# Optimization experiments

Measured on AMD Instinct MI355X. Metric: run time of the kernel, lower is better.

## Reference

```python
import jax, jax.numpy as jnp
import numpy as np

N, C, K, H = 100000, 128, 16, 128
MIX_IN = 2 * C + 1 + C   # x, mean_feat, boundary_score, coord_embed
GATE_IN = 2 * C + 1


def _mlp2(x, w1, b1, w2, b2):
    # Linear -> GELU(exact) -> Linear (dropout=0 at eval)
    return jax.nn.gelu(x @ w1 + b1, approximate=False) @ w2 + b2


def setup_inputs() -> dict:
    key = jax.random.key(0)
    ks = jax.random.split(key, 16)
    s = 0.02
    return {
        "feats": jax.random.normal(ks[0], (N, C), jnp.float32),
        "points": jax.random.normal(ks[1], (N, 3), jnp.float32),
        "neighbors": jax.random.randint(ks[2], (N, K), 0, N, jnp.int64),
        "ln_g": jnp.ones((C,), jnp.float32),
        "ln_b": jnp.zeros((C,), jnp.float32),
        "cp_w1": jax.random.normal(ks[3], (3, H), jnp.float32) * s,
        "cp_b1": jnp.zeros((H,), jnp.float32),
        "cp_w2": jax.random.normal(ks[4], (H, C), jnp.float32) * s,
        "cp_b2": jnp.zeros((C,), jnp.float32),
        "bd_w1": jax.random.normal(ks[5], (2, H), jnp.float32) * s,
        "bd_b1": jnp.zeros((H,), jnp.float32),
        "bd_w2": jax.random.normal(ks[6], (H, 1), jnp.float32) * s,
        "bd_b2": jnp.zeros((1,), jnp.float32),
        "mix_w1": jax.random.normal(ks[7], (MIX_IN, H), jnp.float32) * s,
        "mix_b1": jnp.zeros((H,), jnp.float32),
        "mix_w2": jax.random.normal(ks[8], (H, C), jnp.float32) * s,
        "mix_b2": jnp.zeros((C,), jnp.float32),
        "gate_w1": jax.random.normal(ks[9], (GATE_IN, H), jnp.float32) * s,
        "gate_b1": jnp.zeros((H,), jnp.float32),
        "gate_w2": jax.random.normal(ks[10], (H, C), jnp.float32) * s,
        "gate_b2": jnp.zeros((C,), jnp.float32),
        "out_w": jax.random.normal(ks[11], (C, C), jnp.float32) * s,
        "out_b": jnp.zeros((C,), jnp.float32),
    }


def _forward(feats, points, neighbors, ln_g, ln_b, cp_w1, cp_b1, cp_w2, cp_b2,
             bd_w1, bd_b1, bd_w2, bd_b2, mix_w1, mix_b1, mix_w2, mix_b2,
             gate_w1, gate_b1, gate_w2, gate_b2, out_w, out_b):
    n = feats.shape[0]
    # LayerNorm (eps=1e-5, torch default)
    mu = feats.mean(-1, keepdims=True)
    var = jnp.mean((feats - mu) ** 2, -1, keepdims=True)
    x = (feats - mu) * jax.lax.rsqrt(var + 1e-5) * ln_g + ln_b

    # sanitize neighbors
    valid = ((neighbors >= 0) & (neighbors < n)).astype(x.dtype)  # [N,K]
    safe = jnp.clip(neighbors, 0, n - 1)

    neigh_feats = x[safe]        # [N,K,C]
    neigh_points = points[safe]  # [N,K,3]
    denom = jnp.maximum(valid.sum(1, keepdims=True), 1.0)  # [N,1]
    w = valid[..., None]
    mean_feat = (neigh_feats * w).sum(1) / denom    # [N,C]
    mean_point = (neigh_points * w).sum(1) / denom  # [N,3]

    feat_diff = jnp.linalg.norm(x - mean_feat, axis=-1, keepdims=True)       # [N,1]
    coord_diff = jnp.linalg.norm(points - mean_point, axis=-1, keepdims=True)

    boundary = jax.nn.sigmoid(_mlp2(jnp.concatenate([feat_diff, coord_diff], -1),
                                    bd_w1, bd_b1, bd_w2, bd_b2))  # [N,1]

    # normalize points globally
    centered = points - points.mean(0, keepdims=True)
    scale = jnp.maximum(jnp.abs(centered).max(0, keepdims=True), 1e-6)
    coord_embed = _mlp2(centered / scale, cp_w1, cp_b1, cp_w2, cp_b2)  # [N,C]

    refined = _mlp2(jnp.concatenate([x, mean_feat, boundary, coord_embed], -1),
                    mix_w1, mix_b1, mix_w2, mix_b2)
    gate = jax.nn.sigmoid(_mlp2(jnp.concatenate([x, mean_feat, boundary], -1),
                                gate_w1, gate_b1, gate_w2, gate_b2))
    refined = (gate * refined) @ out_w + out_b
    return feats + refined


def reference(feats, points, neighbors, ln_g, ln_b, cp_w1, cp_b1, cp_w2, cp_b2,
              bd_w1, bd_b1, bd_w2, bd_b2, mix_w1, mix_b1, mix_w2, mix_b2,
              gate_w1, gate_b1, gate_w2, gate_b2, out_w, out_b):
    return _forward(feats, points, neighbors, ln_g, ln_b, cp_w1, cp_b1, cp_w2, cp_b2,
                    bd_w1, bd_b1, bd_w2, bd_b2, mix_w1, mix_b1, mix_w2, mix_b2,
                    gate_w1, gate_b1, gate_w2, gate_b2, out_w, out_b)
```

## Files before the change

### kernel.cpp

```cpp
#include <hip/hip_runtime.h>
#include <math.h>

constexpr int C    = 128;
constexpr int K    = 16;
constexpr int H    = 128;
constexpr int NB2  = 256;
constexpr int WPTS = 32;
constexpr int PB   = 128;
constexpr int HSU  = 68;

constexpr int WT_MIX   = 0;
constexpr int WT_GATE  = 49152;
constexpr int WT_CP2   = 81920;
constexpr int WT_MIX2  = 98304;
constexpr int WT_GATE2 = 114688;
constexpr int WT_OUT   = 131072;
constexpr int WT_TOTAL = 147456;

typedef __attribute__((ext_vector_type(8))) short short8;
typedef __attribute__((ext_vector_type(4))) short short4v;
typedef __attribute__((ext_vector_type(4))) float f32x4;

__device__ __forceinline__ short f2bf(float f) {
    unsigned u = __float_as_uint(f);
    unsigned r = (u + 0x7fffu + ((u >> 16) & 1u)) >> 16;
    return (short)r;
}
__device__ __forceinline__ float bflo(unsigned v) { return __uint_as_float(v << 16); }
__device__ __forceinline__ float bfhi(unsigned v) { return __uint_as_float(v & 0xffff0000u); }
__device__ __forceinline__ float rcpf(float v) { return __builtin_amdgcn_rcpf(v); }

__device__ __forceinline__ float gelu_f(float x) {
    float a = fabsf(x) * 0.70710678118654752440f;
    float t = rcpf(1.0f + 0.3275911f * a);
    float p = t * (0.254829592f + t * (-0.284496736f + t * (1.421413741f
            + t * (-1.453152027f + t * 1.061405429f))));
    float e = __expf(-a * a);
    float er = 1.0f - p * e;
    return 0.5f * x * (1.0f + copysignf(er, x));
}
__device__ __forceinline__ float sigm(float v) { return rcpf(1.0f + __expf(-v)); }

__global__ __launch_bounds__(256) void prep_wt(
    const float* __restrict__ mix_w1, const float* __restrict__ gate_w1,
    const float* __restrict__ cp_w2,  const float* __restrict__ mix_w2,
    const float* __restrict__ gate_w2, const float* __restrict__ out_w,
    short* __restrict__ wt, unsigned* __restrict__ xb_zero_row)
{
    int b = blockIdx.x;
    if (b == 36) {
        if (threadIdx.x < 64) xb_zero_row[threadIdx.x] = 0u;
        return;
    }
    const float* src; int off; int c; bool skip256 = false;
    if (b < 12)      { src = mix_w1;  off = WT_MIX;   c = b;      skip256 = true; }
    else if (b < 20) { src = gate_w1; off = WT_GATE;  c = b - 12; }
    else if (b < 24) { src = cp_w2;   off = WT_CP2;   c = b - 20; }
    else if (b < 28) { src = mix_w2;  off = WT_MIX2;  c = b - 24; }
    else if (b < 32) { src = gate_w2; off = WT_GATE2; c = b - 28; }
    else             { src = out_w;   off = WT_OUT;   c = b - 32; }
    for (int ii = 0; ii < 16; ++ii) {
        int e = ii * 256 + threadIdx.x;
        int j = e & 7, l = (e >> 3) & 63, t = e >> 9;
        int k = c * 32 + ((l >> 4) * 8) + j;
        int nn = t * 16 + (l & 15);
        int kk = (skip256 && k >= 256) ? k + 1 : k;
        wt[off + c * 4096 + e] = f2bf(src[kk * C + nn]);
    }
}

__global__ __launch_bounds__(256) void ln_kernel(
    const float* __restrict__ feats, const float* __restrict__ g,
    const float* __restrict__ b, unsigned* __restrict__ xb, int n)
{
    const int lane = threadIdx.x & 63;
    const int wave = threadIdx.x >> 6;
    const int i = blockIdx.x * 4 + wave;
    if (i >= n) return;
    const float2 f = *(const float2*)(feats + i * C + 2 * lane);
    float s = f.x + f.y;
    #pragma unroll
    for (int o = 32; o > 0; o >>= 1) s += __shfl_xor(s, o, 64);
    const float mu = s * (1.0f / C);
    const float d0 = f.x - mu, d1 = f.y - mu;
    float v = d0 * d0 + d1 * d1;
    #pragma unroll
    for (int o = 32; o > 0; o >>= 1) v += __shfl_xor(v, o, 64);
    const float rs = rsqrtf(v * (1.0f / C) + 1e-5f);
    const float x0 = d0 * rs * g[2 * lane] + b[2 * lane];
    const float x1 = d1 * rs * g[2 * lane + 1] + b[2 * lane + 1];
    unsigned pk = (unsigned short)f2bf(x0) | ((unsigned)(unsigned short)f2bf(x1) << 16);
    xb[(size_t)i * 64 + lane] = pk;
}

__global__ __launch_bounds__(256) void pstat_partial(
    const float* __restrict__ pts, float* __restrict__ partial, int n)
{
    __shared__ float sm[256];
    const int tid = threadIdx.x;
    float s[3] = {0, 0, 0};
    float mn[3] = {1e30f, 1e30f, 1e30f};
    float mx[3] = {-1e30f, -1e30f, -1e30f};
    for (int i = blockIdx.x * blockDim.x + tid; i < n; i += gridDim.x * blockDim.x) {
        #pragma unroll
        for (int c = 0; c < 3; ++c) {
            float v = pts[i * 3 + c];
            s[c] += v; mn[c] = fminf(mn[c], v); mx[c] = fmaxf(mx[c], v);
        }
    }
    for (int q = 0; q < 9; ++q) {
        float v = (q < 3) ? s[q] : (q < 6) ? mn[q - 3] : mx[q - 6];
        sm[tid] = v;
        __syncthreads();
        for (int o = 128; o > 0; o >>= 1) {
            if (tid < o) {
                float a = sm[tid], c = sm[tid + o];
                sm[tid] = (q < 3) ? a + c : (q < 6) ? fminf(a, c) : fmaxf(a, c);
            }
            __syncthreads();
        }
        if (tid == 0) partial[blockIdx.x * 9 + q] = sm[0];
        __syncthreads();
    }
}

__global__ __launch_bounds__(256) void pstat_final(
    const float* __restrict__ partial, float* __restrict__ stats, int n)
{
    __shared__ float sm[256];
    const int tid = threadIdx.x;
    for (int q = 0; q < 9; ++q) {
        float v = partial[tid * 9 + q];
        sm[tid] = v;
        __syncthreads();
        for (int o = 128; o > 0; o >>= 1) {
            if (tid < o) {
                float a = sm[tid], c = sm[tid + o];
                sm[tid] = (q < 3) ? a + c : (q < 6) ? fminf(a, c) : fmaxf(a, c);
            }
            __syncthreads();
        }
        if (tid == 0) sm[q] = sm[0];
        __syncthreads();
    }
    if (tid < 3) {
        float mean = sm[tid] / (float)n;
        float scale = fmaxf(fmaxf(sm[6 + tid] - mean, mean - sm[3 + tid]), 1e-6f);
        stats[tid] = mean;
        stats[3 + tid] = scale;
    }
}

__global__ __launch_bounds__(256, 2) void main_kernel(
    const unsigned* __restrict__ xb, const float* __restrict__ feats,
    const float* __restrict__ points, const int* __restrict__ neighbors,
    const float* __restrict__ stats, const short* __restrict__ wt,
    const float* __restrict__ cp_w1, const float* __restrict__ cp_b1,
    const float* __restrict__ cp_b2,
    const float* __restrict__ bd_w1, const float* __restrict__ bd_b1,
    const float* __restrict__ bd_w2, const float* __restrict__ bd_b2,
    const float* __restrict__ mix_w1, const float* __restrict__ mix_b1,
    const float* __restrict__ mix_b2,
    const float* __restrict__ gate_w1, const float* __restrict__ gate_b1,
    const float* __restrict__ gate_b2,
    const float* __restrict__ out_b,
    float* __restrict__ out, int n)
{
    __shared__ __align__(16) char lds[74752];
    unsigned* mf_s  = (unsigned*)lds;
    unsigned* hid_s = (unsigned*)(lds + 34816);
    float* denom_s  = (float*)(lds + 69632);
    float* mp_s     = denom_s + 128;
    float* pts_s    = mp_s + 384;
    float* cd_s     = pts_s + 512;
    float* bd_s     = cd_s + 128;

    const int tid  = threadIdx.x;
    const int lane = tid & 63;
    const int w    = tid >> 6;
    const int m16  = lane & 15;
    const int h4   = lane >> 4;
    const int i0   = blockIdx.x * PB;
    const int wv32 = w * WPTS;
    const int i0w  = i0 + wv32;
    int* nb_w = (int*)(hid_s + (size_t)wv32 * HSU);

    {
        const int p0 = lane >> 2;
        const int jb = 4 * (lane & 3);
        const int r0 = min(i0w + p0, n - 1);
        const int r1 = min(i0w + 16 + p0, n - 1);
        const int4 A0 = *(const int4*)(neighbors + r0 * K + jb);
        const int4 A1 = *(const int4*)(neighbors + r1 * K + jb);

        const bool b00 = (unsigned)A0.x < (unsigned)n, b01 = (unsigned)A0.y < (unsigned)n;
        const bool b02 = (unsigned)A0.z < (unsigned)n, b03 = (unsigned)A0.w < (unsigned)n;
        const bool b10 = (unsigned)A1.x < (unsigned)n, b11 = (unsigned)A1.y < (unsigned)n;
        const bool b12 = (unsigned)A1.z < (unsigned)n, b13 = (unsigned)A1.w < (unsigned)n;

        *(int4*)&nb_w[4 * lane]       = make_int4(b00 ? A0.x : n, b01 ? A0.y : n,
                                                  b02 ? A0.z : n, b03 ? A0.w : n);
        *(int4*)&nb_w[256 + 4 * lane] = make_int4(b10 ? A1.x : n, b11 ? A1.y : n,
                                                  b12 ? A1.z : n, b13 ? A1.w : n);

        float c0 = (float)((int)b00 + (int)b01 + (int)b02 + (int)b03);
        float c1 = (float)((int)b10 + (int)b11 + (int)b12 + (int)b13);
        c0 += __shfl_xor(c0, 1, 64); c0 += __shfl_xor(c0, 2, 64);
        c1 += __shfl_xor(c1, 1, 64); c1 += __shfl_xor(c1, 2, 64);
        const float d0 = fmaxf(c0, 1.0f), d1 = fmaxf(c1, 1.0f);
        if ((lane & 3) == 0) {
            denom_s[wv32 + p0]      = d0;
            denom_s[wv32 + 16 + p0] = d1;
        }
        const float rd0 = rcpf(d0), rd1 = rcpf(d1);

        const int q00 = b00 ? A0.x : 0, q01 = b01 ? A0.y : 0, q02 = b02 ? A0.z : 0, q03 = b03 ? A0.w : 0;
        const int q10 = b10 ? A1.x : 0, q11 = b11 ? A1.y : 0, q12 = b12 ? A1.z : 0, q13 = b13 ? A1.w : 0;
        const float f00 = b00 ? 1.f : 0.f, f01 = b01 ? 1.f : 0.f, f02 = b02 ? 1.f : 0.f, f03 = b03 ? 1.f : 0.f;
        const float f10 = b10 ? 1.f : 0.f, f11 = b11 ? 1.f : 0.f, f12 = b12 ? 1.f : 0.f, f13 = b13 ? 1.f : 0.f;
        #pragma unroll
        for (int c = 0; c < 3; ++c) {
            float s0 = f00 * points[q00 * 3 + c] + f01 * points[q01 * 3 + c]
                     + f02 * points[q02 * 3 + c] + f03 * points[q03 * 3 + c];
            float s1 = f10 * points[q10 * 3 + c] + f11 * points[q11 * 3 + c]
                     + f12 * points[q12 * 3 + c] + f13 * points[q13 * 3 + c];
            s0 += __shfl_xor(s0, 1, 64); s0 += __shfl_xor(s0, 2, 64);
            s1 += __shfl_xor(s1, 1, 64); s1 += __shfl_xor(s1, 2, 64);
            if ((lane & 3) == 0) {
                mp_s[(wv32 + p0) * 3 + c]      = s0 * rd0;
                mp_s[(wv32 + 16 + p0) * 3 + c] = s1 * rd1;
            }
        }
    }

    if (lane < WPTS) {
        const int ipp = min(i0w + lane, n - 1);
        const float pv0 = points[ipp * 3 + 0];
        const float pv1 = points[ipp * 3 + 1];
        const float pv2 = points[ipp * 3 + 2];
        const float e0 = pv0 - mp_s[(wv32 + lane) * 3 + 0];
        const float e1 = pv1 - mp_s[(wv32 + lane) * 3 + 1];
        const float e2 = pv2 - mp_s[(wv32 + lane) * 3 + 2];
        cd_s[wv32 + lane] = sqrtf(e0 * e0 + e1 * e1 + e2 * e2);
        pts_s[(wv32 + lane) * 4 + 0] = (pv0 - stats[0]) * rcpf(stats[3]);
        pts_s[(wv32 + lane) * 4 + 1] = (pv1 - stats[1]) * rcpf(stats[4]);
        pts_s[(wv32 + lane) * 4 + 2] = (pv2 - stats[2]) * rcpf(stats[5]);
    }

    const float bw_fa = bd_w1[lane],     bw_fb = bd_w1[64 + lane];
    const float bw_ca = bd_w1[H + lane], bw_cb = bd_w1[H + 64 + lane];
    const float bb1a  = bd_b1[lane],     bb1b  = bd_b1[64 + lane];
    const float bw2a  = bd_w2[lane],     bw2b  = bd_w2[64 + lane];
    const float bb2   = bd_b2[0];

    for (int p = 0; p < WPTS; ++p) {
        const int* nbp = nb_w + p * K;
        float fx = 0.0f, fy = 0.0f;
        #pragma unroll
        for (int k = 0; k < K; ++k) {
            const int idx = nbp[k];
            const unsigned v = xb[(size_t)idx * 64 + lane];
            fx += bflo(v); fy += bfhi(v);
        }
        const float rden = rcpf(denom_s[wv32 + p]);
        const float mfx = fx * rden, mfy = fy * rden;
        mf_s[(wv32 + p) * HSU + lane] =
            (unsigned)(unsigned short)f2bf(mfx) | ((unsigned)(unsigned short)f2bf(mfy) << 16);
        const int ipp = min(i0w + p, n - 1);
        const unsigned xv = xb[(size_t)ipp * 64 + lane];
        const float dx = bflo(xv) - mfx, dy = bfhi(xv) - mfy;
        float ss = dx * dx + dy * dy;
        #pragma unroll
        for (int o = 32; o > 0; o >>= 1) ss += __shfl_xor(ss, o, 64);
        const float fd = sqrtf(ss);
        const float cd = cd_s[wv32 + p];
        float s = gelu_f(fd * bw_fa + cd * bw_ca + bb1a) * bw2a
                + gelu_f(fd * bw_fb + cd * bw_cb + bb1b) * bw2b;
        #pragma unroll
        for (int o = 32; o > 0; o >>= 1) s += __shfl_xor(s, o, 64);
        if (lane == 0) bd_s[wv32 + p] = sigm(s + bb2);
    }

    const int pr0 = wv32 + m16, pr1 = wv32 + 16 + m16;
    const int ig0 = i0 + pr0,   ig1 = i0 + pr1;
    const int ip0 = min(ig0, n - 1), ip1 = min(ig1, n - 1);
    const unsigned* xr0  = xb + (size_t)ip0 * 64;
    const unsigned* xr1  = xb + (size_t)ip1 * 64;
    const unsigned* mfr0 = mf_s + pr0 * HSU;
    const unsigned* mfr1 = mf_s + pr1 * HSU;
    unsigned* hr0 = hid_s + pr0 * HSU;
    unsigned* hr1 = hid_s + pr1 * HSU;

    {
        const float px0 = pts_s[pr0 * 4], py0 = pts_s[pr0 * 4 + 1], pz0 = pts_s[pr0 * 4 + 2];
        const float px1 = pts_s[pr1 * 4], py1 = pts_s[pr1 * 4 + 1], pz1 = pts_s[pr1 * 4 + 2];
        f32x4 a0[8], a1[8];
        #pragma unroll
        for (int t = 0; t < 8; ++t) { a0[t] = (f32x4)0.0f; a1[t] = (f32x4)0.0f; }
        #pragma unroll
        for (int c = 0; c < 4; ++c) {
            short8 af0, af1;
            #pragma unroll
            for (int j = 0; j < 8; ++j) {
                const int hh = c * 32 + h4 * 8 + j;
                const float wa = cp_w1[hh], wb = cp_w1[H + hh], wc2 = cp_w1[2 * H + hh];
                const float bb = cp_b1[hh];
                af0[j] = f2bf(gelu_f(bb + px0 * wa + py0 * wb + pz0 * wc2));
                af1[j] = f2bf(gelu_f(bb + px1 * wa + py1 * wb + pz1 * wc2));
            }
            const short* wcp = wt + WT_CP2 + c * 4096 + lane * 8;
            #pragma unroll
            for (int t = 0; t < 8; ++t) {
                const short8 wf = *(const short8*)(wcp + t * 512);
                a0[t] = __builtin_amdgcn_mfma_f32_16x16x32_bf16(wf, af0, a0[t], 0, 0, 0);
                a1[t] = __builtin_amdgcn_mfma_f32_16x16x32_bf16(wf, af1, a1[t], 0, 0, 0);
            }
        }
        #pragma unroll
        for (int t = 0; t < 8; ++t) {
            const f32x4 bb = *(const f32x4*)(cp_b2 + t * 16 + h4 * 4);
            const f32x4 v0 = a0[t] + bb, v1 = a1[t] + bb;
            short4v pk0, pk1;
            #pragma unroll
            for (int r = 0; r < 4; ++r) { pk0[r] = f2bf(v0[r]); pk1[r] = f2bf(v1[r]); }
            *(short4v*)((short*)hr0 + t * 16 + h4 * 4) = pk0;
            *(short4v*)((short*)hr1 + t * 16 + h4 * 4) = pk1;
        }
    }

    const float bdp0 = bd_s[pr0], bdp1 = bd_s[pr1];

    {
        f32x4 a0[8], a1[8];
        #pragma unroll
        for (int t = 0; t < 8; ++t) { a0[t] = (f32x4)0.0f; a1[t] = (f32x4)0.0f; }
        #pragma unroll
        for (int c = 0; c < 12; ++c) {
            short8 af0, af1;
            if (c < 4) {
                af0 = *(const short8*)(xr0 + c * 16 + h4 * 4);
                af1 = *(const short8*)(xr1 + c * 16 + h4 * 4);
            } else if (c < 8) {
                af0 = *(const short8*)(mfr0 + (c - 4) * 16 + h4 * 4);
                af1 = *(const short8*)(mfr1 + (c - 4) * 16 + h4 * 4);
            } else {
                af0 = *(const short8*)(hr0 + (c - 8) * 16 + h4 * 4);
                af1 = *(const short8*)(hr1 + (c - 8) * 16 + h4 * 4);
            }
            const short* wmc = wt + WT_MIX + c * 4096 + lane * 8;
            #pragma unroll
            for (int t = 0; t < 8; ++t) {
                const short8 wf = *(const short8*)(wmc + t * 512);
                a0[t] = __builtin_amdgcn_mfma_f32_16x16x32_bf16(wf, af0, a0[t], 0, 0, 0);
                a1[t] = __builtin_amdgcn_mfma_f32_16x16x32_bf16(wf, af1, a1[t], 0, 0, 0);
            }
        }
        #pragma unroll
        for (int t = 0; t < 8; ++t) {
            const int col = t * 16 + h4 * 4;
            const f32x4 wb = *(const f32x4*)(mix_w1 + 256 * C + col);
            const f32x4 bb = *(const f32x4*)(mix_b1 + col);
            const f32x4 v0 = a0[t] + bdp0 * wb + bb;
            const f32x4 v1 = a1[t] + bdp1 * wb + bb;
            short4v pk0, pk1;
            #pragma unroll
            for (int r = 0; r < 4; ++r) { pk0[r] = f2bf(gelu_f(v0[r])); pk1[r] = f2bf(gelu_f(v1[r])); }
            *(short4v*)((short*)hr0 + col) = pk0;
            *(short4v*)((short*)hr1 + col) = pk1;
        }
    }

    f32x4 rf0[8], rf1[8];
    {
        #pragma unroll
        for (int t = 0; t < 8; ++t) { rf0[t] = (f32x4)0.0f; rf1[t] = (f32x4)0.0f; }
        #pragma unroll
        for (int c = 0; c < 4; ++c) {
            const short8 af0 = *(const short8*)(hr0 + c * 16 + h4 * 4);
            const short8 af1 = *(const short8*)(hr1 + c * 16 + h4 * 4);
            const short* wmc = wt + WT_MIX2 + c * 4096 + lane * 8;
            #pragma unroll
            for (int t = 0; t < 8; ++t) {
                const short8 wf = *(const short8*)(wmc + t * 512);
                rf0[t] = __builtin_amdgcn_mfma_f32_16x16x32_bf16(wf, af0, rf0[t], 0, 0, 0);
                rf1[t] = __builtin_amdgcn_mfma_f32_16x16x32_bf16(wf, af1, rf1[t], 0, 0, 0);
            }
        }
        #pragma unroll
        for (int t = 0; t < 8; ++t) {
            const f32x4 bb = *(const f32x4*)(mix_b2 + t * 16 + h4 * 4);
            rf0[t] += bb; rf1[t] += bb;
        }
    }

    {
        f32x4 a0[8], a1[8];
        #pragma unroll
        for (int t = 0; t < 8; ++t) { a0[t] = (f32x4)0.0f; a1[t] = (f32x4)0.0f; }
        #pragma unroll
        for (int c = 0; c < 8; ++c) {
            short8 af0, af1;
            if (c < 4) {
                af0 = *(const short8*)(xr0 + c * 16 + h4 * 4);
                af1 = *(const short8*)(xr1 + c * 16 + h4 * 4);
            } else {
                af0 = *(const short8*)(mfr0 + (c - 4) * 16 + h4 * 4);
                af1 = *(const short8*)(mfr1 + (c - 4) * 16 + h4 * 4);
            }
            const short* wgc = wt + WT_GATE + c * 4096 + lane * 8;
            #pragma unroll
            for (int t = 0; t < 8; ++t) {
                const short8 wf = *(const short8*)(wgc + t * 512);
                a0[t] = __builtin_amdgcn_mfma_f32_16x16x32_bf16(wf, af0, a0[t], 0, 0, 0);
                a1[t] = __builtin_amdgcn_mfma_f32_16x16x32_bf16(wf, af1, a1[t], 0, 0, 0);
            }
        }
        #pragma unroll
        for (int t = 0; t < 8; ++t) {
            const int col = t * 16 + h4 * 4;
            const f32x4 wb = *(const f32x4*)(gate_w1 + 256 * C + col);
            const f32x4 bb = *(const f32x4*)(gate_b1 + col);
            const f32x4 v0 = a0[t] + bdp0 * wb + bb;
            const f32x4 v1 = a1[t] + bdp1 * wb + bb;
            short4v pk0, pk1;
            #pragma unroll
            for (int r = 0; r < 4; ++r) { pk0[r] = f2bf(gelu_f(v0[r])); pk1[r] = f2bf(gelu_f(v1[r])); }
            *(short4v*)((short*)hr0 + col) = pk0;
            *(short4v*)((short*)hr1 + col) = pk1;
        }
    }

    {
        f32x4 a0[8], a1[8];
        #pragma unroll
        for (int t = 0; t < 8; ++t) { a0[t] = (f32x4)0.0f; a1[t] = (f32x4)0.0f; }
        #pragma unroll
        for (int c = 0; c < 4; ++c) {
            const short8 af0 = *(const short8*)(hr0 + c * 16 + h4 * 4);
            const short8 af1 = *(const short8*)(hr1 + c * 16 + h4 * 4);
            const short* wgc = wt + WT_GATE2 + c * 4096 + lane * 8;
            #pragma unroll
            for (int t = 0; t < 8; ++t) {
                const short8 wf = *(const short8*)(wgc + t * 512);
                a0[t] = __builtin_amdgcn_mfma_f32_16x16x32_bf16(wf, af0, a0[t], 0, 0, 0);
                a1[t] = __builtin_amdgcn_mfma_f32_16x16x32_bf16(wf, af1, a1[t], 0, 0, 0);
            }
        }
        #pragma unroll
        for (int t = 0; t < 8; ++t) {
            const int col = t * 16 + h4 * 4;
            const f32x4 bb = *(const f32x4*)(gate_b2 + col);
            short4v pk0, pk1;
            #pragma unroll
            for (int r = 0; r < 4; ++r) {
                pk0[r] = f2bf(sigm(a0[t][r] + bb[r]) * rf0[t][r]);
                pk1[r] = f2bf(sigm(a1[t][r] + bb[r]) * rf1[t][r]);
            }
            *(short4v*)((short*)hr0 + col) = pk0;
            *(short4v*)((short*)hr1 + col) = pk1;
        }
    }

    {
        f32x4 a0[8], a1[8];
        #pragma unroll
        for (int t = 0; t < 8; ++t) { a0[t] = (f32x4)0.0f; a1[t] = (f32x4)0.0f; }
        #pragma unroll
        for (int c = 0; c < 4; ++c) {
            const short8 af0 = *(const short8*)(hr0 + c * 16 + h4 * 4);
            const short8 af1 = *(const short8*)(hr1 + c * 16 + h4 * 4);
            const short* woc = wt + WT_OUT + c * 4096 + lane * 8;
            #pragma unroll
            for (int t = 0; t < 8; ++t) {
                const short8 wf = *(const short8*)(woc + t * 512);
                a0[t] = __builtin_amdgcn_mfma_f32_16x16x32_bf16(wf, af0, a0[t], 0, 0, 0);
                a1[t] = __builtin_amdgcn_mfma_f32_16x16x32_bf16(wf, af1, a1[t], 0, 0, 0);
            }
        }
        #pragma unroll
        for (int t = 0; t < 8; ++t) {
            const int col = t * 16 + h4 * 4;
            const f32x4 bb = *(const f32x4*)(out_b + col);
            const f32x4 fv0 = *(const f32x4*)(feats + (size_t)ip0 * C + col);
            const f32x4 fv1 = *(const f32x4*)(feats + (size_t)ip1 * C + col);
            const f32x4 v0 = a0[t] + bb + fv0;
            const f32x4 v1 = a1[t] + bb + fv1;
            if (ig0 < n) *(f32x4*)(out + (size_t)ig0 * C + col) = v0;
            if (ig1 < n) *(f32x4*)(out + (size_t)ig1 * C + col) = v1;
        }
    }
}

extern "C" void kernel_launch(void* const* d_in, const int* in_sizes, int n_in,
                              void* d_out, int out_size, void* d_ws, size_t ws_size,
                              hipStream_t stream)
{
    const float* feats     = (const float*)d_in[0];
    const float* points    = (const float*)d_in[1];
    const int*   neighbors = (const int*)d_in[2];
    const float* ln_g      = (const float*)d_in[3];
    const float* ln_b      = (const float*)d_in[4];
    const float* cp_w1     = (const float*)d_in[5];
    const float* cp_b1     = (const float*)d_in[6];
    const float* cp_w2     = (const float*)d_in[7];
    const float* cp_b2     = (const float*)d_in[8];
    const float* bd_w1     = (const float*)d_in[9];
    const float* bd_b1     = (const float*)d_in[10];
    const float* bd_w2     = (const float*)d_in[11];
    const float* bd_b2     = (const float*)d_in[12];
    const float* mix_w1    = (const float*)d_in[13];
    const float* mix_b1    = (const float*)d_in[14];
    const float* mix_w2    = (const float*)d_in[15];
    const float* mix_b2    = (const float*)d_in[16];
    const float* gate_w1   = (const float*)d_in[17];
    const float* gate_b1   = (const float*)d_in[18];
    const float* gate_w2   = (const float*)d_in[19];
    const float* gate_b2   = (const float*)d_in[20];
    const float* out_w     = (const float*)d_in[21];
    const float* out_b     = (const float*)d_in[22];
    float* out = (float*)d_out;
    (void)n_in; (void)out_size; (void)ws_size;

    const int n = in_sizes[0] / C;

    char* base = (char*)d_ws;
    unsigned* xb   = (unsigned*)base;
    short* wt      = (short*)(base + (size_t)(n + 1) * 256);
    float* partial = (float*)((char*)wt + (size_t)WT_TOTAL * 2);
    float* stats   = partial + NB2 * 9;

    prep_wt<<<37, 256, 0, stream>>>(mix_w1, gate_w1, cp_w2, mix_w2, gate_w2, out_w,
                                    wt, xb + (size_t)n * 64);
    ln_kernel<<<(n + 3) / 4, 256, 0, stream>>>(feats, ln_g, ln_b, xb, n);
    pstat_partial<<<NB2, 256, 0, stream>>>(points, partial, n);
    pstat_final<<<1, 256, 0, stream>>>(partial, stats, n);
    main_kernel<<<(n + PB - 1) / PB, 256, 0, stream>>>(
        xb, feats, points, neighbors, stats, wt,
        cp_w1, cp_b1, cp_b2, bd_w1, bd_b1, bd_w2, bd_b2,
        mix_w1, mix_b1, mix_b2, gate_w1, gate_b1, gate_b2,
        out_b, out, n);
}
```

Before: 375.1 us.

## Gather neighbor features in FP8 e5m2 with prefetch and padded point array

LayerNorm now also writes an 8-bit e5m2 copy of the normalized features, and the neighbor-mean gather reads it instead of the bf16 copy. This halves the bytes fetched per neighbor row. The gather loop is restructured so each half-wave handles one point, and the next point's 16 neighbor loads are prefetched into registers while the current point is reduced. Points are also repacked into a padded float4 array so neighbor coordinates come in as single vector loads, and the coordinate-difference computation is folded into the setup. The cost is a much coarser mean_feat (e5m2 has only 2 mantissa bits), which risks tolerance failures, plus higher register pressure from the prefetch buffers.

```diff
diff --git a/kernel.cpp b/kernel.cpp
--- a/kernel.cpp
+++ b/kernel.cpp
@@ -29,6 +29,17 @@
 __device__ __forceinline__ float bflo(unsigned v) { return __uint_as_float(v << 16); }
 __device__ __forceinline__ float bfhi(unsigned v) { return __uint_as_float(v & 0xffff0000u); }
 __device__ __forceinline__ float rcpf(float v) { return __builtin_amdgcn_rcpf(v); }
+
+__device__ __forceinline__ float e5m2f(unsigned b) {
+    union { unsigned short u; _Float16 h; } cv;
+    cv.u = (unsigned short)((b & 0xFFu) << 8);
+    return (float)cv.h;
+}
+__device__ __forceinline__ unsigned f2e5m2(float x) {
+    union { _Float16 h; unsigned short u; } cv;
+    cv.h = (_Float16)x;
+    return ((unsigned)cv.u + 0x7Fu + ((cv.u >> 8) & 1u)) >> 8;
+}
 
 __device__ __forceinline__ float gelu_f(float x) {
     float a = fabsf(x) * 0.70710678118654752440f;
@@ -45,11 +56,27 @@
     const float* __restrict__ mix_w1, const float* __restrict__ gate_w1,
     const float* __restrict__ cp_w2,  const float* __restrict__ mix_w2,
     const float* __restrict__ gate_w2, const float* __restrict__ out_w,
-    short* __restrict__ wt, unsigned* __restrict__ xb_zero_row)
+    const float* __restrict__ points,
+    short* __restrict__ wt, unsigned* __restrict__ xb_zero,
+    unsigned* __restrict__ xg_zero, float* __restrict__ pts4, int n)
 {
     int b = blockIdx.x;
     if (b == 36) {
-        if (threadIdx.x < 64) xb_zero_row[threadIdx.x] = 0u;
+        if (threadIdx.x < 64) xb_zero[threadIdx.x] = 0u;
+        else if (threadIdx.x < 96) xg_zero[threadIdx.x - 64] = 0u;
+        return;
+    }
+    if (b >= 37) {
+        int i = (b - 37) * 256 + threadIdx.x;
+        if (i < n) {
+            pts4[i * 4 + 0] = points[i * 3 + 0];
+            pts4[i * 4 + 1] = points[i * 3 + 1];
+            pts4[i * 4 + 2] = points[i * 3 + 2];
+            pts4[i * 4 + 3] = 0.0f;
+        } else if (i == n) {
+            pts4[i * 4 + 0] = 0.0f; pts4[i * 4 + 1] = 0.0f;
+            pts4[i * 4 + 2] = 0.0f; pts4[i * 4 + 3] = 0.0f;
+        }
         return;
     }
     const float* src; int off; int c; bool skip256 = false;
@@ -71,7 +98,8 @@
 
 __global__ __launch_bounds__(256) void ln_kernel(
     const float* __restrict__ feats, const float* __restrict__ g,
-    const float* __restrict__ b, unsigned* __restrict__ xb, int n)
+    const float* __restrict__ b, unsigned* __restrict__ xb,
+    unsigned short* __restrict__ xg, int n)
 {
     const int lane = threadIdx.x & 63;
     const int wave = threadIdx.x >> 6;
@@ -89,8 +117,10 @@
     const float rs = rsqrtf(v * (1.0f / C) + 1e-5f);
     const float x0 = d0 * rs * g[2 * lane] + b[2 * lane];
     const float x1 = d1 * rs * g[2 * lane + 1] + b[2 * lane + 1];
-    unsigned pk = (unsigned short)f2bf(x0) | ((unsigned)(unsigned short)f2bf(x1) << 16);
-    xb[(size_t)i * 64 + lane] = pk;
+    xb[(size_t)i * 64 + lane] =
+        (unsigned)(unsigned short)f2bf(x0) | ((unsigned)(unsigned short)f2bf(x1) << 16);
+    xg[(size_t)i * 64 + lane] =
+        (unsigned short)(f2e5m2(x0) | (f2e5m2(x1) << 8));
 }
 
 __global__ __launch_bounds__(256) void pstat_partial(
@@ -152,8 +182,9 @@
 }
 
 __global__ __launch_bounds__(256, 2) void main_kernel(
-    const unsigned* __restrict__ xb, const float* __restrict__ feats,
-    const float* __restrict__ points, const int* __restrict__ neighbors,
+    const unsigned* __restrict__ xb, const unsigned* __restrict__ xg,
+    const float* __restrict__ pts4, const float* __restrict__ feats,
+    const int* __restrict__ neighbors,
     const float* __restrict__ stats, const short* __restrict__ wt,
     const float* __restrict__ cp_w1, const float* __restrict__ cp_b1,
     const float* __restrict__ cp_b2,
@@ -166,12 +197,11 @@
     const float* __restrict__ out_b,
     float* __restrict__ out, int n)
 {
-    __shared__ __align__(16) char lds[74752];
+    __shared__ __align__(16) char lds[73216];
     unsigned* mf_s  = (unsigned*)lds;
     unsigned* hid_s = (unsigned*)(lds + 34816);
     float* denom_s  = (float*)(lds + 69632);
-    float* mp_s     = denom_s + 128;
-    float* pts_s    = mp_s + 384;
+    float* pts_s    = denom_s + 128;
     float* cd_s     = pts_s + 512;
     float* bd_s     = cd_s + 128;
 
@@ -190,21 +220,23 @@
         const int jb = 4 * (lane & 3);
         const int r0 = min(i0w + p0, n - 1);
         const int r1 = min(i0w + 16 + p0, n - 1);
-        const int4 A0 = *(const int4*)(neighbors + r0 * K + jb);
-        const int4 A1 = *(const int4*)(neighbors + r1 * K + jb);
-
-        const bool b00 = (unsigned)A0.x < (unsigned)n, b01 = (unsigned)A0.y < (unsigned)n;
-        const bool b02 = (unsigned)A0.z < (unsigned)n, b03 = (unsigned)A0.w < (unsigned)n;
-        const bool b10 = (unsigned)A1.x < (unsigned)n, b11 = (unsigned)A1.y < (unsigned)n;
-        const bool b12 = (unsigned)A1.z < (unsigned)n, b13 = (unsigned)A1.w < (unsigned)n;
-
-        *(int4*)&nb_w[4 * lane]       = make_int4(b00 ? A0.x : n, b01 ? A0.y : n,
-                                                  b02 ? A0.z : n, b03 ? A0.w : n);
-        *(int4*)&nb_w[256 + 4 * lane] = make_int4(b10 ? A1.x : n, b11 ? A1.y : n,
-                                                  b12 ? A1.z : n, b13 ? A1.w : n);
-
-        float c0 = (float)((int)b00 + (int)b01 + (int)b02 + (int)b03);
-        float c1 = (float)((int)b10 + (int)b11 + (int)b12 + (int)b13);
+        const int4 A0 = *(const int4*)(neighbors + (size_t)r0 * K + jb);
+        const int4 A1 = *(const int4*)(neighbors + (size_t)r1 * K + jb);
+
+        const int q00 = ((unsigned)A0.x < (unsigned)n) ? A0.x : n;
+        const int q01 = ((unsigned)A0.y < (unsigned)n) ? A0.y : n;
+        const int q02 = ((unsigned)A0.z < (unsigned)n) ? A0.z : n;
+        const int q03 = ((unsigned)A0.w < (unsigned)n) ? A0.w : n;
+        const int q10 = ((unsigned)A1.x < (unsigned)n) ? A1.x : n;
+        const int q11 = ((unsigned)A1.y < (unsigned)n) ? A1.y : n;
+        const int q12 = ((unsigned)A1.z < (unsigned)n) ? A1.z : n;
+        const int q13 = ((unsigned)A1.w < (unsigned)n) ? A1.w : n;
+
+        *(int4*)&nb_w[4 * lane]       = make_int4(q00, q01, q02, q03);
+        *(int4*)&nb_w[256 + 4 * lane] = make_int4(q10, q11, q12, q13);
+
+        float c0 = (float)((q00 != n) + (q01 != n) + (q02 != n) + (q03 != n));
+        float c1 = (float)((q10 != n) + (q11 != n) + (q12 != n) + (q13 != n));
         c0 += __shfl_xor(c0, 1, 64); c0 += __shfl_xor(c0, 2, 64);
         c1 += __shfl_xor(c1, 1, 64); c1 += __shfl_xor(c1, 2, 64);
         const float d0 = fmaxf(c0, 1.0f), d1 = fmaxf(c1, 1.0f);
@@ -212,73 +244,97 @@
             denom_s[wv32 + p0]      = d0;
             denom_s[wv32 + 16 + p0] = d1;
         }
-        const float rd0 = rcpf(d0), rd1 = rcpf(d1);
-
-        const int q00 = b00 ? A0.x : 0, q01 = b01 ? A0.y : 0, q02 = b02 ? A0.z : 0, q03 = b03 ? A0.w : 0;
-        const int q10 = b10 ? A1.x : 0, q11 = b11 ? A1.y : 0, q12 = b12 ? A1.z : 0, q13 = b13 ? A1.w : 0;
-        const float f00 = b00 ? 1.f : 0.f, f01 = b01 ? 1.f : 0.f, f02 = b02 ? 1.f : 0.f, f03 = b03 ? 1.f : 0.f;
-        const float f10 = b10 ? 1.f : 0.f, f11 = b11 ? 1.f : 0.f, f12 = b12 ? 1.f : 0.f, f13 = b13 ? 1.f : 0.f;
+
+        f32x4 s0 = *(const f32x4*)(pts4 + 4 * q00);
+        s0 += *(const f32x4*)(pts4 + 4 * q01);
+        s0 += *(const f32x4*)(pts4 + 4 * q02);
+        s0 += *(const f32x4*)(pts4 + 4 * q03);
+        f32x4 s1 = *(const f32x4*)(pts4 + 4 * q10);
+        s1 += *(const f32x4*)(pts4 + 4 * q11);
+        s1 += *(const f32x4*)(pts4 + 4 * q12);
+        s1 += *(const f32x4*)(pts4 + 4 * q13);
         #pragma unroll
         for (int c = 0; c < 3; ++c) {
-            float s0 = f00 * points[q00 * 3 + c] + f01 * points[q01 * 3 + c]
-                     + f02 * points[q02 * 3 + c] + f03 * points[q03 * 3 + c];
-            float s1 = f10 * points[q10 * 3 + c] + f11 * points[q11 * 3 + c]
-                     + f12 * points[q12 * 3 + c] + f13 * points[q13 * 3 + c];
-            s0 += __shfl_xor(s0, 1, 64); s0 += __shfl_xor(s0, 2, 64);
-            s1 += __shfl_xor(s1, 1, 64); s1 += __shfl_xor(s1, 2, 64);
-            if ((lane & 3) == 0) {
-                mp_s[(wv32 + p0) * 3 + c]      = s0 * rd0;
-                mp_s[(wv32 + 16 + p0) * 3 + c] = s1 * rd1;
-            }
+            s0[c] += __shfl_xor(s0[c], 1, 64); s0[c] += __shfl_xor(s0[c], 2, 64);
+            s1[c] += __shfl_xor(s1[c], 1, 64); s1[c] += __shfl_xor(s1[c], 2, 64);
+        }
+        if ((lane & 3) == 0) {
+            const float rd0 = rcpf(d0), rd1 = rcpf(d1);
+            const f32x4 pv0 = *(const f32x4*)(pts4 + 4 * r0);
+            const f32x4 pv1 = *(const f32x4*)(pts4 + 4 * r1);
+            const float e00 = pv0[0] - s0[0] * rd0, e01 = pv0[1] - s0[1] * rd0, e02 = pv0[2] - s0[2] * rd0;
+            const float e10 = pv1[0] - s1[0] * rd1, e11 = pv1[1] - s1[1] * rd1, e12 = pv1[2] - s1[2] * rd1;
+            cd_s[wv32 + p0]      = sqrtf(e00 * e00 + e01 * e01 + e02 * e02);
+            cd_s[wv32 + 16 + p0] = sqrtf(e10 * e10 + e11 * e11 + e12 * e12);
         }
     }
 
     if (lane < WPTS) {
         const int ipp = min(i0w + lane, n - 1);
-        const float pv0 = points[ipp * 3 + 0];
-        const float pv1 = points[ipp * 3 + 1];
-        const float pv2 = points[ipp * 3 + 2];
-        const float e0 = pv0 - mp_s[(wv32 + lane) * 3 + 0];
-        const float e1 = pv1 - mp_s[(wv32 + lane) * 3 + 1];
-        const float e2 = pv2 - mp_s[(wv32 + lane) * 3 + 2];
-        cd_s[wv32 + lane] = sqrtf(e0 * e0 + e1 * e1 + e2 * e2);
-        pts_s[(wv32 + lane) * 4 + 0] = (pv0 - stats[0]) * rcpf(stats[3]);
-        pts_s[(wv32 + lane) * 4 + 1] = (pv1 - stats[1]) * rcpf(stats[4]);
-        pts_s[(wv32 + lane) * 4 + 2] = (pv2 - stats[2]) * rcpf(stats[5]);
-    }
-
-    const float bw_fa = bd_w1[lane],     bw_fb = bd_w1[64 + lane];
-    const float bw_ca = bd_w1[H + lane], bw_cb = bd_w1[H + 64 + lane];
-    const float bb1a  = bd_b1[lane],     bb1b  = bd_b1[64 + lane];
-    const float bw2a  = bd_w2[lane],     bw2b  = bd_w2[64 + lane];
-    const float bb2   = bd_b2[0];
-
-    for (int p = 0; p < WPTS; ++p) {
-        const int* nbp = nb_w + p * K;
-        float fx = 0.0f, fy = 0.0f;
+        const f32x4 pv = *(const f32x4*)(pts4 + 4 * ipp);
+        pts_s[(wv32 + lane) * 4 + 0] = (pv[0] - stats[0]) * rcpf(stats[3]);
+        pts_s[(wv32 + lane) * 4 + 1] = (pv[1] - stats[1]) * rcpf(stats[4]);
+        pts_s[(wv32 + lane) * 4 + 2] = (pv[2] - stats[2]) * rcpf(stats[5]);
+    }
+
+    {
+        const int ul   = lane & 31;
+        const int half = lane >> 5;
+        float w1f[4], w1c[4], b1v[4], w2v[4];
+        #pragma unroll
+        for (int j = 0; j < 4; ++j) {
+            int u = ul + 32 * j;
+            w1f[j] = bd_w1[u]; w1c[j] = bd_w1[H + u];
+            b1v[j] = bd_b1[u]; w2v[j] = bd_w2[u];
+        }
+        const float bb2 = bd_b2[0];
+
+        unsigned cur[16], nxt[16];
         #pragma unroll
         for (int k = 0; k < K; ++k) {
-            const int idx = nbp[k];
-            const unsigned v = xb[(size_t)idx * 64 + lane];
-            fx += bflo(v); fy += bfhi(v);
-        }
-        const float rden = rcpf(denom_s[wv32 + p]);
-        const float mfx = fx * rden, mfy = fy * rden;
-        mf_s[(wv32 + p) * HSU + lane] =
-            (unsigned)(unsigned short)f2bf(mfx) | ((unsigned)(unsigned short)f2bf(mfy) << 16);
-        const int ipp = min(i0w + p, n - 1);
-        const unsigned xv = xb[(size_t)ipp * 64 + lane];
-        const float dx = bflo(xv) - mfx, dy = bfhi(xv) - mfy;
-        float ss = dx * dx + dy * dy;
-        #pragma unroll
-        for (int o = 32; o > 0; o >>= 1) ss += __shfl_xor(ss, o, 64);
-        const float fd = sqrtf(ss);
-        const float cd = cd_s[wv32 + p];
-        float s = gelu_f(fd * bw_fa + cd * bw_ca + bb1a) * bw2a
-                + gelu_f(fd * bw_fb + cd * bw_cb + bb1b) * bw2b;
-        #pragma unroll
-        for (int o = 32; o > 0; o >>= 1) s += __shfl_xor(s, o, 64);
-        if (lane == 0) bd_s[wv32 + p] = sigm(s + bb2);
+            const int r = nb_w[half * K + k];
+            cur[k] = xg[(size_t)r * 32 + ul];
+        }
+        for (int pr = 0; pr < 16; ++pr) {
+            if (pr < 15) {
+                #pragma unroll
+                for (int k = 0; k < K; ++k) {
+                    const int r = nb_w[((pr + 1) * 2 + half) * K + k];
+                    nxt[k] = xg[(size_t)r * 32 + ul];
+                }
+            }
+            float f0 = 0, f1 = 0, f2 = 0, f3 = 0;
+            #pragma unroll
+            for (int k = 0; k < K; ++k) {
+                const unsigned u = cur[k];
+                f0 += e5m2f(u); f1 += e5m2f(u >> 8);
+                f2 += e5m2f(u >> 16); f3 += e5m2f(u >> 24);
+            }
+            const int p = 2 * pr + half;
+            const float rden = rcpf(denom_s[wv32 + p]);
+            f0 *= rden; f1 *= rden; f2 *= rden; f3 *= rden;
+            short4v pk; pk[0] = f2bf(f0); pk[1] = f2bf(f1); pk[2] = f2bf(f2); pk[3] = f2bf(f3);
+            *(short4v*)((short*)mf_s + (size_t)(wv32 + p) * (HSU * 2) + ul * 4) = pk;
+
+            const int ipp = min(i0w + p, n - 1);
+            const uint2 xv = *(const uint2*)(xb + (size_t)ipp * 64 + 2 * ul);
+            const float d0 = bflo(xv.x) - f0, d1 = bfhi(xv.x) - f1;
+            const float d2 = bflo(xv.y) - f2, d3 = bfhi(xv.y) - f3;
+            float ss = d0 * d0 + d1 * d1 + d2 * d2 + d3 * d3;
+            #pragma unroll
+            for (int o = 16; o > 0; o >>= 1) ss += __shfl_xor(ss, o, 64);
+            const float fd = sqrtf(ss);
+            const float cd = cd_s[wv32 + p];
+            float s = 0.0f;
+            #pragma unroll
+            for (int j = 0; j < 4; ++j)
+                s += gelu_f(fd * w1f[j] + cd * w1c[j] + b1v[j]) * w2v[j];
+            #pragma unroll
+            for (int o = 16; o > 0; o >>= 1) s += __shfl_xor(s, o, 64);
+            if (ul == 0) bd_s[wv32 + p] = sigm(s + bb2);
+            #pragma unroll
+            for (int k = 0; k < K; ++k) cur[k] = nxt[k];
+        }
     }
 
     const int pr0 = wv32 + m16, pr1 = wv32 + 16 + m16;
@@ -524,18 +580,22 @@
     const int n = in_sizes[0] / C;
 
     char* base = (char*)d_ws;
-    unsigned* xb   = (unsigned*)base;
-    short* wt      = (short*)(base + (size_t)(n + 1) * 256);
-    float* partial = (float*)((char*)wt + (size_t)WT_TOTAL * 2);
-    float* stats   = partial + NB2 * 9;
-
-    prep_wt<<<37, 256, 0, stream>>>(mix_w1, gate_w1, cp_w2, mix_w2, gate_w2, out_w,
-                                    wt, xb + (size_t)n * 64);
-    ln_kernel<<<(n + 3) / 4, 256, 0, stream>>>(feats, ln_g, ln_b, xb, n);
+    unsigned* xb        = (unsigned*)base;
+    unsigned short* xg  = (unsigned short*)(base + (size_t)(n + 1) * 256);
+    float* pts4         = (float*)(base + (size_t)(n + 1) * 256 + (size_t)(n + 1) * 128);
+    short* wt           = (short*)((char*)pts4 + (size_t)(n + 1) * 16);
+    float* partial      = (float*)((char*)wt + (size_t)WT_TOTAL * 2);
+    float* stats        = partial + NB2 * 9;
+
+    const int prep_blocks = 37 + (n + 256) / 256;
+    prep_wt<<<prep_blocks, 256, 0, stream>>>(
+        mix_w1, gate_w1, cp_w2, mix_w2, gate_w2, out_w, points,
+        wt, xb + (size_t)n * 64, (unsigned*)(xg + (size_t)n * 64), pts4, n);
+    ln_kernel<<<(n + 3) / 4, 256, 0, stream>>>(feats, ln_g, ln_b, xb, xg, n);
     pstat_partial<<<NB2, 256, 0, stream>>>(points, partial, n);
     pstat_final<<<1, 256, 0, stream>>>(partial, stats, n);
     main_kernel<<<(n + PB - 1) / PB, 256, 0, stream>>>(
-        xb, feats, points, neighbors, stats, wt,
+        xb, (const unsigned*)xg, pts4, feats, neighbors, stats, wt,
         cp_w1, cp_b1, cp_b2, bd_w1, bd_b1, bd_w2, bd_b2,
         mix_w1, mix_b1, mix_b2, gate_w1, gate_b1, gate_b2,
         out_b, out, n);
```

New measurement: 338.7 us. 1.11x faster.
